# Optimization experiments

Hardware: AMD Instinct MI355X
Metric: run time of the kernel (lower is better)

## Reference

```python
import jax, jax.numpy as jnp
import numpy as np

N_HEADS = 16
HEAD_DIM = 128
ROPE_BASE = 50000.0
EPS = 1e-06


def _rotate_half(x):
    half = x.shape[-1] // 2
    return jnp.concatenate([-x[..., half:], x[..., :half]], axis=-1)


def _rms_norm(x, w):
    rms = jnp.sqrt(jnp.mean(x * x, axis=-1, keepdims=True) + EPS)
    return w * (x / rms)


def _rope_tables(n, dim, dtype):
    inv_freq = 1.0 / (ROPE_BASE ** (jnp.arange(0, dim, 2, dtype=jnp.float32) / dim))
    t = jnp.arange(n, dtype=jnp.float32)
    freqs = jnp.outer(t, inv_freq)          # [n, dim/2]
    emb = jnp.concatenate([freqs, freqs], axis=-1)  # [n, dim]
    return jnp.cos(emb).astype(dtype), jnp.sin(emb).astype(dtype)


def setup_inputs() -> dict:
    key = jax.random.key(0)
    ks = jax.random.split(key, 5)
    B, n, d = 2, 2048, 2048
    inner = N_HEADS * HEAD_DIM
    s = 1.0 / np.sqrt(d)
    return {
        "x": jax.random.normal(ks[0], (B, n, d), jnp.float32),
        "Wq": jax.random.normal(ks[1], (d, inner), jnp.float32) * s,
        "Wk": jax.random.normal(ks[2], (d, inner), jnp.float32) * s,
        "Wv": jax.random.normal(ks[3], (d, inner), jnp.float32) * s,
        "Wo": jax.random.normal(ks[4], (inner, d), jnp.float32) * s,
        "qn_w": jnp.ones((inner,), jnp.float32),
        "kn_w": jnp.ones((inner,), jnp.float32),
    }


def reference(x, Wq, Wk, Wv, Wo, qn_w, kn_w):
    B, n, d = x.shape
    # QKV projections (no bias)
    q = x @ Wq
    k = x @ Wk
    v = x @ Wv
    # QK RMSNorm over full inner_dim (as in the torch module)
    q = _rms_norm(q, qn_w)
    k = _rms_norm(k, kn_w)
    # [B, H, n, Dh]
    q = q.reshape(B, n, N_HEADS, HEAD_DIM).transpose(0, 2, 1, 3)
    k = k.reshape(B, n, N_HEADS, HEAD_DIM).transpose(0, 2, 1, 3)
    v = v.reshape(B, n, N_HEADS, HEAD_DIM).transpose(0, 2, 1, 3)
    # RoPE (rotary_dim == head_dim -> full rotation)
    cos, sin = _rope_tables(n, HEAD_DIM, x.dtype)  # [n, Dh]
    cos = cos[None, None]
    sin = sin[None, None]
    q = q * cos + _rotate_half(q) * sin
    k = k * cos + _rotate_half(k) * sin
    # Causal SDPA
    scale = 1.0 / np.sqrt(HEAD_DIM)
    scores = jnp.einsum("bhqd,bhkd->bhqk", q, k) * scale
    causal = jnp.tril(jnp.ones((n, n), dtype=bool))
    scores = jnp.where(causal, scores, jnp.finfo(scores.dtype).min)
    attn = jax.nn.softmax(scores, axis=-1)
    out = jnp.einsum("bhqk,bhkd->bhqd", attn, v)
    out = out.transpose(0, 2, 1, 3).reshape(B, n, N_HEADS * HEAD_DIM)
    return out @ Wo
```

## Files before the change

kernel.cpp:

```cpp
#include <hip/hip_runtime.h>

typedef unsigned short u16;
typedef unsigned int u32;
typedef __attribute__((ext_vector_type(8))) short short8;
typedef __attribute__((ext_vector_type(4))) float f32x4;
typedef __attribute__((ext_vector_type(16))) float f32x16;
typedef __attribute__((ext_vector_type(4))) u32 u32x4;

typedef __attribute__((address_space(3))) unsigned int as3u32;
typedef __attribute__((address_space(1))) unsigned int as1u32;

__device__ __forceinline__ void gld16(void* lds, const void* g) {
    __builtin_amdgcn_global_load_lds((as1u32*)(void*)g, (as3u32*)lds, 16, 0, 0);
}

__device__ inline float bf2f(u16 u) {
    u32 v = ((u32)u) << 16;
    return __builtin_bit_cast(float, v);
}
__device__ inline u16 f2bf(float f) {
    u32 u = __builtin_bit_cast(u32, f);
    u32 r = u + 0x7FFF + ((u >> 16) & 1);
    return (u16)(r >> 16);
}
__device__ __forceinline__ u32 cvtpk_bf16(float lo, float hi) {
    u32 r;
    asm("v_cvt_pk_bf16_f32 %0, %1, %2" : "=v"(r) : "v"(lo), "v"(hi));
    return r;
}
__device__ inline void unpack8(uint4 v, float* f) {
    u32 a[4] = {v.x, v.y, v.z, v.w};
#pragma unroll
    for (int i = 0; i < 4; ++i) {
        f[2 * i]     = bf2f((u16)(a[i] & 0xffff));
        f[2 * i + 1] = bf2f((u16)(a[i] >> 16));
    }
}

__global__ __launch_bounds__(256) void prep_all(const float* __restrict__ x,
                                                const float* __restrict__ Wq,
                                                const float* __restrict__ Wk,
                                                const float* __restrict__ Wv,
                                                const float* __restrict__ Wo,
                                                u16* __restrict__ Xbf,
                                                u16* __restrict__ Wtqkv,
                                                u16* __restrict__ Wot,
                                                float* __restrict__ cosb,
                                                float* __restrict__ sinb) {
    __shared__ float tile[64][65];
    const int bx = blockIdx.x;
    const int t = threadIdx.x;
    if (bx < 4096) {
        int i = (bx * 256 + t) * 8;
        float4 a = *(const float4*)&x[i];
        float4 b = *(const float4*)&x[i + 4];
        u16 o[8];
        o[0] = f2bf(a.x); o[1] = f2bf(a.y); o[2] = f2bf(a.z); o[3] = f2bf(a.w);
        o[4] = f2bf(b.x); o[5] = f2bf(b.y); o[6] = f2bf(b.z); o[7] = f2bf(b.w);
        *(uint4*)&Xbf[i] = *(uint4*)o;
        return;
    }
    if (bx < 8192) {
        const int i = bx - 4096;
        const int z = i >> 10, rem = i & 1023;
        const int n0 = (rem & 31) * 64, k0 = (rem >> 5) * 64;
        const float* in;
        u16* out;
        switch (z) {
            case 0:  in = Wq; out = Wtqkv;            break;
            case 1:  in = Wk; out = Wtqkv + 4194304;  break;
            case 2:  in = Wv; out = Wtqkv + 8388608;  break;
            default: in = Wo; out = Wot;              break;
        }
        const int lr = t >> 4, lc = (t & 15) * 4;
#pragma unroll
        for (int rep = 0; rep < 4; ++rep) {
            float4 v = *(const float4*)&in[(size_t)(k0 + rep * 16 + lr) * 2048 + n0 + lc];
            tile[rep * 16 + lr][lc + 0] = v.x;
            tile[rep * 16 + lr][lc + 1] = v.y;
            tile[rep * 16 + lr][lc + 2] = v.z;
            tile[rep * 16 + lr][lc + 3] = v.w;
        }
        __syncthreads();
        const int nr = t >> 3, kc = (t & 7) * 8;
#pragma unroll
        for (int rep = 0; rep < 2; ++rep) {
            const int n = rep * 32 + nr;
            u16 o[8];
#pragma unroll
            for (int e = 0; e < 8; ++e) o[e] = f2bf(tile[kc + e][n]);
            *(uint4*)&out[(size_t)(n0 + n) * 2048 + k0 + kc] = *(uint4*)o;
        }
        return;
    }
    {
        int idx = (bx - 8192) * 256 + t;
        int pos = idx >> 6, i = idx & 63;
        float invf = __expf(-(float)i * (10.819778284410283f / 64.0f));
        float a = (float)pos * invf;
        cosb[idx] = cosf(a);
        sinb[idx] = sinf(a);
    }
}

template <bool BF16OUT>
__global__ __launch_bounds__(256) void gemm_bt(const u16* __restrict__ A,
                                               const u16* __restrict__ Bt,
                                               void* __restrict__ Cv,
                                               int M, int N, int K) {
    __shared__ u16 As[2][128][64];
    __shared__ u16 Bs[2][128][64];
    const int bm = blockIdx.y, bn = blockIdx.x;
    const int tid = threadIdx.x;
    const int lane = tid & 63, w = tid >> 6;
    const int wm = (w >> 1) * 64, wn = (w & 1) * 64;
    const int lrow = lane & 15;
    const int sw = (lane & 7) << 4;
    const int srl = lane >> 3;
    const int ssw = ((lane & 7) * 16) ^ (srl << 4);
    const char* AB = (const char*)A;
    const char* BB = (const char*)Bt;
    const int NT = K >> 6;
    f32x4 acc[4][4] = {};

    const char* Ab[4];
    const char* Bb[4];
#pragma unroll
    for (int i = 0; i < 4; ++i) {
        const int rb = i * 32 + w * 8;
        Ab[i] = AB + ((size_t)(bm * 128 + rb + srl) * K) * 2 + ssw;
        Bb[i] = BB + ((size_t)(bn * 128 + rb + srl) * K) * 2 + ssw;
    }

#pragma unroll
    for (int i = 0; i < 4; ++i) {
        const int rb = i * 32 + w * 8;
        gld16(&As[0][rb][0], Ab[i]);
        gld16(&Bs[0][rb][0], Bb[i]);
    }

    for (int t = 0; t < NT; ++t) {
        const int buf = t & 1;
        __syncthreads();
        if (t + 1 < NT) {
            const size_t ko = (size_t)(t + 1) * 128;
#pragma unroll
            for (int i = 0; i < 4; ++i) {
                const int rb = i * 32 + w * 8;
                gld16(&As[buf ^ 1][rb][0], Ab[i] + ko);
                gld16(&Bs[buf ^ 1][rb][0], Bb[i] + ko);
            }
        }
        const char* AsB = (const char*)&As[buf][0][0];
        const char* BsB = (const char*)&Bs[buf][0][0];
#pragma unroll
        for (int kk = 0; kk < 2; ++kk) {
            const int cb = (kk * 64 + (lane >> 4) * 16) ^ sw;
            short8 af[4], bf_[4];
#pragma unroll
            for (int i = 0; i < 4; ++i)
                af[i] = *(const short8*)(AsB + (wm + i * 16 + lrow) * 128 + cb);
#pragma unroll
            for (int j = 0; j < 4; ++j)
                bf_[j] = *(const short8*)(BsB + (wn + j * 16 + lrow) * 128 + cb);
            __builtin_amdgcn_s_setprio(1);
#pragma unroll
            for (int i = 0; i < 4; ++i)
#pragma unroll
                for (int j = 0; j < 4; ++j)
                    acc[i][j] = __builtin_amdgcn_mfma_f32_16x16x32_bf16(af[i], bf_[j], acc[i][j], 0, 0, 0);
            __builtin_amdgcn_s_setprio(0);
        }
    }
    const int crow = (lane >> 4) * 4, ccol = lane & 15;
#pragma unroll
    for (int i = 0; i < 4; ++i)
#pragma unroll
        for (int j = 0; j < 4; ++j)
#pragma unroll
            for (int r = 0; r < 4; ++r) {
                size_t off = (size_t)(bm * 128 + wm + i * 16 + crow + r) * N +
                             (size_t)(bn * 128 + wn + j * 16 + ccol);
                if (BF16OUT) ((u16*)Cv)[off] = f2bf(acc[i][j][r]);
                else         ((float*)Cv)[off] = acc[i][j][r];
            }
}

__global__ __launch_bounds__(256) void norm_rope_v(const u16* __restrict__ qkv,
                                                   const float* __restrict__ qw,
                                                   const float* __restrict__ kw,
                                                   const float* __restrict__ cosb,
                                                   const float* __restrict__ sinb,
                                                   u16* __restrict__ Qout,
                                                   u16* __restrict__ Kout,
                                                   u16* __restrict__ Vt) {
    __shared__ __align__(16) char smem[17408];
    const int bx = blockIdx.x;
    const int t = threadIdx.x;
    if (bx < 4096) {
        float* qf = (float*)smem;
        float* kf = (float*)(smem + 8192);
        __shared__ float red[8];
        const int r = bx;
        const int b = r >> 11, pos = r & 2047;
        const u16* row = qkv + (size_t)r * 6144;
        uint4 qv = *(const uint4*)&row[t * 8];
        uint4 kv = *(const uint4*)&row[2048 + t * 8];
        float qe[8], ke[8];
        unpack8(qv, qe);
        unpack8(kv, ke);
        float sq = 0.f, sk = 0.f;
#pragma unroll
        for (int e = 0; e < 8; ++e) {
            qf[t * 8 + e] = qe[e];
            kf[t * 8 + e] = ke[e];
            sq += qe[e] * qe[e];
            sk += ke[e] * ke[e];
        }
#pragma unroll
        for (int msk = 1; msk < 64; msk <<= 1) {
            sq += __shfl_xor(sq, msk);
            sk += __shfl_xor(sk, msk);
        }
        if ((t & 63) == 0) { red[t >> 6] = sq; red[4 + (t >> 6)] = sk; }
        __syncthreads();
        float ssq = red[0] + red[1] + red[2] + red[3];
        float ssk = red[4] + red[5] + red[6] + red[7];
        const float invq = 0.12751946f / sqrtf(ssq * (1.f / 2048.f) + 1e-6f);
        const float invk = 1.0f / sqrtf(ssk * (1.f / 2048.f) + 1e-6f);
        const float* ct = cosb + pos * 64;
        const float* st = sinb + pos * 64;
        u16 qo[8], ko[8];
#pragma unroll
        for (int e = 0; e < 8; ++e) {
            int c = t * 8 + e;
            int jl = c & 127;
            int hb = c & ~127;
            int jj = jl & 63;
            float cs = ct[jj], sn = st[jj];
            int pair = hb + ((jl < 64) ? jl + 64 : jl - 64);
            float sgn = (jl < 64) ? -1.f : 1.f;
            float xq = qf[c] * qw[c], pq = qf[pair] * qw[pair];
            float xk = kf[c] * kw[c], pk = kf[pair] * kw[pair];
            qo[e] = f2bf((xq * cs + sgn * pq * sn) * invq);
            ko[e] = f2bf((xk * cs + sgn * pk * sn) * invk);
        }
        const int h = (t * 8) >> 7;
        const int j0 = (t * 8) & 127;
        size_t o = ((size_t)(b * 16 + h) * 2048 + pos) * 128 + j0;
        *(uint4*)&Qout[o] = *(uint4*)qo;
        *(uint4*)&Kout[o] = *(uint4*)ko;
        return;
    }
    {
        u16 (*tile)[136] = (u16(*)[136])smem;
        const int i = bx - 4096;
        const int pt = i & 31, bh = i >> 5;
        const int b = bh >> 4, h = bh & 15;
        const int pos0 = pt * 64;
        const int p = t >> 4, jc = (t & 15) * 8;
#pragma unroll
        for (int rep = 0; rep < 4; ++rep)
            *(uint4*)&tile[rep * 16 + p][jc] =
                *(const uint4*)&qkv[(size_t)(b * 2048 + pos0 + rep * 16 + p) * 6144 + 4096 + h * 128 + jc];
        __syncthreads();
        const int j = t >> 3, pc = (t & 7) * 8;
#pragma unroll
        for (int rep = 0; rep < 4; ++rep) {
            const int jj = rep * 32 + j;
            u16 tmp[8];
#pragma unroll
            for (int e = 0; e < 8; ++e) tmp[e] = tile[pc + e][jj];
            *(uint4*)&Vt[((size_t)bh * 128 + jj) * 2048 + pos0 + pc] = *(uint4*)tmp;
        }
    }
}

__global__ __launch_bounds__(256, 2) void attn_fwd(const u16* __restrict__ Qr,
                                                   const u16* __restrict__ Kr,
                                                   const u16* __restrict__ Vt,
                                                   u16* __restrict__ O) {
    __shared__ u16 Ks[2][64][128];
    __shared__ u16 VsT[2][128][64];
    const int bx = blockIdx.x;
    const int g = bx >> 3;
    const int bh = (bx & 7) + 8 * (g & 3);
    const int qt = (g < 32) ? (15 - (g >> 2)) : ((g >> 2) - 8);
    const int tid = threadIdx.x;
    const int lane = tid & 63, w = tid >> 6;
    const int ql = lane & 31, h = lane >> 5;
    const char* KhB = (const char*)(Kr + (size_t)bh * 2048 * 128);
    const char* VhB = (const char*)(Vt + (size_t)bh * 128 * 2048);
    const u16* Qh = Qr + (size_t)bh * 2048 * 128;
    const int b = bh >> 4, hh = bh & 15;
    const int krl = lane >> 4;
    const int ksc = (lane & 15) * 16;
    const int vrl = lane >> 3;
    const int vsc = (lane & 7) * 16;
    const int swz = (ql & 7) << 4;

    const int q0w = qt * 128 + w * 32;
    const int qg = q0w + ql;
    short8 qb[8];
#pragma unroll
    for (int s = 0; s < 8; ++s)
        qb[s] = *(const short8*)&Qh[(size_t)qg * 128 + s * 16 + h * 8];

    f32x16 ot[4] = {};
    float m = -3e38f, ls = 0.f;
    const int kend = qt * 128 + 128;

#pragma unroll
    for (int j = 0; j < 4; ++j) {
        const int krb = w * 16 + j * 4;
        const int kr = krb + krl;
        gld16(&Ks[0][krb][0], KhB + (size_t)kr * 256 + (ksc ^ ((kr & 7) << 4)));
        const int vrb = w * 32 + j * 8;
        const int vr = vrb + vrl;
        gld16(&VsT[0][vrb][0], VhB + (size_t)vr * 4096 + (vsc ^ ((vr & 7) << 4)));
    }

    for (int k0 = 0; k0 < kend; k0 += 64) {
        const int buf = (k0 >> 6) & 1;
        __syncthreads();
        if (k0 + 64 < kend) {
            const int kn = k0 + 64;
#pragma unroll
            for (int j = 0; j < 4; ++j) {
                const int krb = w * 16 + j * 4;
                const int kr = krb + krl;
                gld16(&Ks[buf ^ 1][krb][0],
                      KhB + (size_t)(kn + kr) * 256 + (ksc ^ ((kr & 7) << 4)));
                const int vrb = w * 32 + j * 8;
                const int vr = vrb + vrl;
                gld16(&VsT[buf ^ 1][vrb][0],
                      VhB + (size_t)vr * 4096 + (size_t)kn * 2 + (vsc ^ ((vr & 7) << 4)));
            }
        }
        const char* KsB = (const char*)&Ks[buf][0][0];
        const char* VsB = (const char*)&VsT[buf][0][0];

        f32x16 st[2] = {};
#pragma unroll
        for (int s = 0; s < 8; ++s) {
            short8 kf0 = *(const short8*)(KsB + (size_t)ql * 256 + ((s * 32 + 16 * h) ^ swz));
            short8 kf1 = *(const short8*)(KsB + (size_t)(32 + ql) * 256 + ((s * 32 + 16 * h) ^ swz));
            st[0] = __builtin_amdgcn_mfma_f32_32x32x16_bf16(kf0, qb[s], st[0], 0, 0, 0);
            st[1] = __builtin_amdgcn_mfma_f32_32x32x16_bf16(kf1, qb[s], st[1], 0, 0, 0);
        }

        if (k0 + 64 > q0w) {
#pragma unroll
            for (int T = 0; T < 2; ++T)
#pragma unroll
                for (int reg = 0; reg < 16; ++reg) {
                    int c = k0 + 32 * T + (reg & 3) + 8 * (reg >> 2) + 4 * h;
                    if (c > qg) st[T][reg] = -1e30f;
                }
        }

        float mx;
        {
            float vm[16];
#pragma unroll
            for (int r = 0; r < 16; ++r) vm[r] = fmaxf(st[0][r], st[1][r]);
            float m4[4];
#pragma unroll
            for (int r = 0; r < 4; ++r)
                m4[r] = fmaxf(fmaxf(vm[r], vm[4 + r]), fmaxf(vm[8 + r], vm[12 + r]));
            mx = fmaxf(fmaxf(m4[0], m4[1]), fmaxf(m4[2], m4[3]));
            mx = fmaxf(mx, __shfl_xor(mx, 32));
        }

        if (__any(mx > m + 8.f)) {
            float mn = fmaxf(m, mx);
            float corr = exp2f(m - mn);
            m = mn;
            ls *= corr;
#pragma unroll
            for (int td = 0; td < 4; ++td)
#pragma unroll
                for (int reg = 0; reg < 16; ++reg) ot[td][reg] *= corr;
        }

        float ps;
        {
#pragma unroll
            for (int T = 0; T < 2; ++T)
#pragma unroll
                for (int reg = 0; reg < 16; ++reg)
                    st[T][reg] = exp2f(st[T][reg] - m);
            float vs[16];
#pragma unroll
            for (int r = 0; r < 16; ++r) vs[r] = st[0][r] + st[1][r];
            float s4[4];
#pragma unroll
            for (int r = 0; r < 4; ++r)
                s4[r] = (vs[r] + vs[4 + r]) + (vs[8 + r] + vs[12 + r]);
            ps = (s4[0] + s4[1]) + (s4[2] + s4[3]);
            ps += __shfl_xor(ps, 32);
        }
        ls += ps;

#pragma unroll
        for (int T = 0; T < 2; ++T) {
            u32 c[4][2];
#pragma unroll
            for (int mm = 0; mm < 4; ++mm) {
                c[mm][0] = cvtpk_bf16(st[T][4 * mm + 0], st[T][4 * mm + 1]);
                c[mm][1] = cvtpk_bf16(st[T][4 * mm + 2], st[T][4 * mm + 3]);
            }
#pragma unroll
            for (int i = 0; i < 2; ++i) {
                const int ks = 2 * T + i;
                u32 a0 = c[2 * i][0], b0 = c[2 * i + 1][0];
                u32 a1 = c[2 * i][1], b1 = c[2 * i + 1][1];
                asm volatile("v_permlane32_swap_b32 %0, %1" : "+v"(a0), "+v"(b0));
                asm volatile("v_permlane32_swap_b32 %0, %1" : "+v"(a1), "+v"(b1));
                u32x4 pw = {a0, a1, b0, b1};
                short8 pf = __builtin_bit_cast(short8, pw);
#pragma unroll
                for (int td = 0; td < 4; ++td) {
                    short8 vf = *(const short8*)(VsB + (size_t)(32 * td + ql) * 128 +
                                                 ((32 * ks + 16 * h) ^ swz));
                    ot[td] = __builtin_amdgcn_mfma_f32_32x32x16_bf16(vf, pf, ot[td], 0, 0, 0);
                }
            }
        }
    }

    const float inv = 1.0f / ls;
    const size_t base = ((size_t)b * 2048 + qg) * 2048 + (size_t)hh * 128;
#pragma unroll
    for (int td = 0; td < 4; ++td)
#pragma unroll
        for (int g2 = 0; g2 < 4; ++g2) {
            ushort4 o4;
            o4.x = f2bf(ot[td][4 * g2 + 0] * inv);
            o4.y = f2bf(ot[td][4 * g2 + 1] * inv);
            o4.z = f2bf(ot[td][4 * g2 + 2] * inv);
            o4.w = f2bf(ot[td][4 * g2 + 3] * inv);
            *(ushort4*)&O[base + 32 * td + 8 * g2 + 4 * h] = o4;
        }
}

extern "C" void kernel_launch(void* const* d_in, const int* in_sizes, int n_in,
                              void* d_out, int out_size, void* d_ws, size_t ws_size,
                              hipStream_t stream) {
    const float* x   = (const float*)d_in[0];
    const float* Wq  = (const float*)d_in[1];
    const float* Wk  = (const float*)d_in[2];
    const float* Wv  = (const float*)d_in[3];
    const float* Wo  = (const float*)d_in[4];
    const float* qnw = (const float*)d_in[5];
    const float* knw = (const float*)d_in[6];

    const size_t MB = 1ull << 20;
    char* ws = (char*)d_ws;
    u16* Xbf    = (u16*)(ws + 0);
    u16* Qr     = (u16*)(ws + 0);
    u16* Wtqkv  = (u16*)(ws + 16 * MB);
    u16* Wot    = (u16*)(ws + 40 * MB);
    u16* QKV    = (u16*)(ws + 48 * MB);
    u16* AOut   = (u16*)(ws + 48 * MB);
    float* cosb = (float*)(ws + 96 * MB);
    float* sinb = (float*)(ws + 96 * MB + 524288);
    u16* Kr     = (u16*)(ws + 97 * MB);
    u16* Vt     = (u16*)(ws + 113 * MB);

    prep_all<<<8704, 256, 0, stream>>>(x, Wq, Wk, Wv, Wo, Xbf, Wtqkv, Wot, cosb, sinb);

    gemm_bt<true><<<dim3(48, 32), 256, 0, stream>>>(Xbf, Wtqkv, (void*)QKV, 4096, 6144, 2048);

    norm_rope_v<<<5120, 256, 0, stream>>>(QKV, qnw, knw, cosb, sinb, Qr, Kr, Vt);

    attn_fwd<<<512, 256, 0, stream>>>(Qr, Kr, Vt, AOut);

    gemm_bt<false><<<dim3(16, 32), 256, 0, stream>>>(AOut, Wot, d_out, 4096, 2048, 2048);
}
```

Before: 264.5 us.

## Add 256x256-tile 512-thread GEMM with XCD-aware block mapping for QKV projection

Replaces the 128x128-tile QKV projection GEMM with a new kernel that uses 256x256 output tiles, 8 waves per block and one block per CU. It keeps a double-buffered pipeline of K-tiles loaded directly into LDS, with loads spread across eight phases per iteration, and remaps block indices so adjacent tiles land on the same XCD. The larger tile is meant to raise arithmetic intensity and cut global and L2 traffic. In exchange it uses 128KB of LDS, runs at lower occupancy, and writes bf16 results with scalar per-element stores.

```diff
diff --git a/kernel.cpp b/kernel.cpp
--- a/kernel.cpp
+++ b/kernel.cpp
@@ -101,6 +101,123 @@
         cosb[idx] = cosf(a);
         sinb[idx] = sinf(a);
     }
+}
+
+__global__ __launch_bounds__(512, 1) void gemm256(const u16* __restrict__ A,
+                                                  const u16* __restrict__ Bt,
+                                                  u16* __restrict__ C,
+                                                  int M, int N, int K) {
+    __shared__ u16 As[2][256][64];
+    __shared__ u16 Bs[2][256][64];
+    const int NI = K >> 7;
+    const int cpx = gridDim.x >> 3;
+    const int wg = (blockIdx.x & 7) * cpx + (blockIdx.x >> 3);
+    const int gm = M >> 8;
+    const int bn = wg / gm, bm = wg % gm;
+    const int tid = threadIdx.x;
+    const int lane = tid & 63, w = tid >> 6;
+    const int wr = w >> 2, wc = w & 3;
+    const int lrow = lane & 15;
+    const int sw = (lane & 7) << 4;
+    const int sswc = ((lane & 7) * 16) ^ ((lane >> 3) << 4);
+    const size_t Kb = (size_t)K * 2;
+    const char* aThr = (const char*)A +
+        (size_t)(bm * 256 + ((w & 3) << 3) + (lane >> 3) + ((w >> 2) << 7)) * Kb + sswc;
+    const char* bThr = (const char*)Bt +
+        (size_t)(bn * 256 + (w << 3) + (lane >> 3)) * Kb + sswc;
+    const int aDr = ((w & 3) << 3) + ((w >> 2) << 7);
+    const int bDr = (w << 3);
+
+#define STAGE_A(bf, q, tile) gld16(&As[bf][32 * (q) + aDr][0], \
+        aThr + (size_t)(32 * (q)) * Kb + (size_t)(tile) * 128)
+#define STAGE_B(bf, u, tile) gld16(&Bs[bf][64 * (u) + bDr][0], \
+        bThr + (size_t)(64 * (u)) * Kb + (size_t)(tile) * 128)
+
+    f32x4 acc[8][4] = {};
+
+#pragma unroll
+    for (int u = 0; u < 4; ++u) STAGE_B(0, u, 0);
+#pragma unroll
+    for (int q = 0; q < 4; ++q) STAGE_A(0, q, 0);
+#pragma unroll
+    for (int u = 0; u < 4; ++u) STAGE_B(1, u, 1);
+#pragma unroll
+    for (int q = 0; q < 4; ++q) STAGE_A(1, q, 1);
+    asm volatile("s_waitcnt vmcnt(6)" ::: "memory");
+    asm volatile("s_barrier" ::: "memory");
+
+    for (int it = 0; it < NI; ++it) {
+        const bool more = (it + 1 < NI);
+        const int te2 = 2 * it + 2, to2 = 2 * it + 3;
+        short8 bfr[4][2];
+#pragma unroll
+        for (int ph = 0; ph < 8; ++ph) {
+            const int tb = ph >> 2;
+            const int q = ph & 3;
+            const char* AsB = (const char*)&As[tb][0][0];
+            short8 afr[2][2];
+#pragma unroll
+            for (int e = 0; e < 2; ++e)
+#pragma unroll
+                for (int kh = 0; kh < 2; ++kh)
+                    afr[e][kh] = *(const short8*)(AsB +
+                        (wr * 128 + (2 * q + e) * 16 + lrow) * 128 +
+                        ((kh * 64 + (lane >> 4) * 16) ^ sw));
+            if (q == 0) {
+                const char* BsB = (const char*)&Bs[tb][0][0];
+#pragma unroll
+                for (int fn = 0; fn < 4; ++fn)
+#pragma unroll
+                    for (int kh = 0; kh < 2; ++kh)
+                        bfr[fn][kh] = *(const short8*)(BsB +
+                            (wc * 64 + fn * 16 + lrow) * 128 +
+                            ((kh * 64 + (lane >> 4) * 16) ^ sw));
+            }
+            asm volatile("s_waitcnt lgkmcnt(0)" ::: "memory");
+            if (more) {
+                if (ph == 0) { STAGE_B(0, 0, te2); STAGE_B(0, 1, te2); }
+                if (ph == 1) { STAGE_B(0, 2, te2); STAGE_B(0, 3, te2); }
+                if (ph == 2) { STAGE_A(0, 0, te2); STAGE_A(0, 1, te2); }
+                if (ph == 3) { STAGE_A(0, 2, te2); STAGE_A(0, 3, te2); }
+                if (ph == 4) { STAGE_B(1, 0, to2); STAGE_B(1, 1, to2); }
+                if (ph == 5) { STAGE_B(1, 2, to2); STAGE_B(1, 3, to2); }
+                if (ph == 6) { STAGE_A(1, 0, to2); STAGE_A(1, 1, to2); }
+                if (ph == 7) { STAGE_A(1, 2, to2); STAGE_A(1, 3, to2); }
+            }
+            asm volatile("s_barrier" ::: "memory");
+            __builtin_amdgcn_s_setprio(1);
+#pragma unroll
+            for (int e = 0; e < 2; ++e)
+#pragma unroll
+                for (int fn = 0; fn < 4; ++fn)
+#pragma unroll
+                    for (int kh = 0; kh < 2; ++kh)
+                        acc[2 * q + e][fn] = __builtin_amdgcn_mfma_f32_16x16x32_bf16(
+                            afr[e][kh], bfr[fn][kh], acc[2 * q + e][fn], 0, 0, 0);
+            __builtin_amdgcn_s_setprio(0);
+            if (ph == 3) {
+                if (more) asm volatile("s_waitcnt vmcnt(6)" ::: "memory");
+                else      asm volatile("s_waitcnt vmcnt(0)" ::: "memory");
+            }
+            if (ph == 7 && more)
+                asm volatile("s_waitcnt vmcnt(6)" ::: "memory");
+            asm volatile("s_barrier" ::: "memory");
+        }
+    }
+#undef STAGE_A
+#undef STAGE_B
+
+    const int crow = (lane >> 4) * 4, ccol = lane & 15;
+#pragma unroll
+    for (int fm = 0; fm < 8; ++fm)
+#pragma unroll
+        for (int fn = 0; fn < 4; ++fn)
+#pragma unroll
+            for (int r = 0; r < 4; ++r) {
+                size_t off = (size_t)(bm * 256 + wr * 128 + fm * 16 + crow + r) * N +
+                             (size_t)(bn * 256 + wc * 64 + fn * 16 + ccol);
+                C[off] = f2bf(acc[fm][fn][r]);
+            }
 }
 
 template <bool BF16OUT>
@@ -470,7 +587,7 @@
 
     prep_all<<<8704, 256, 0, stream>>>(x, Wq, Wk, Wv, Wo, Xbf, Wtqkv, Wot, cosb, sinb);
 
-    gemm_bt<true><<<dim3(48, 32), 256, 0, stream>>>(Xbf, Wtqkv, (void*)QKV, 4096, 6144, 2048);
+    gemm256<<<384, 512, 0, stream>>>(Xbf, Wtqkv, QKV, 4096, 6144, 2048);
 
     norm_rope_v<<<5120, 256, 0, stream>>>(QKV, qnw, knw, cosb, sinb, Qr, Kr, Vt);
 
```

Measured after the change: 279.2 us. 5.5% more time.
